# Kernel optimization log

Measured on AMD Instinct MI355X. Metric: run time of the kernel, lower is better.

Reference implementation:

```python
import jax, jax.numpy as jnp
import numpy as np

N_HEAD = 16
E = 1024
B, T = 2, 2048


def setup_inputs() -> dict:
    key = jax.random.key(0)
    ks = jax.random.split(key, 5)
    s = 1.0 / np.sqrt(E)
    return {
        "x": jax.random.normal(ks[0], (B, T, E), dtype=jnp.float32),
        "w_qkv": jax.random.normal(ks[1], (E, 3 * E), dtype=jnp.float32) * s,
        "b_qkv": jnp.zeros((3 * E,), dtype=jnp.float32),
        "w_proj": jax.random.normal(ks[2], (E, E), dtype=jnp.float32) * s,
        "b_proj": jnp.zeros((E,), dtype=jnp.float32),
    }


def reference(x, w_qkv, b_qkv, w_proj, b_proj):
    Bsz, Tlen, Emb = x.shape
    hd = Emb // N_HEAD
    qkv = x @ w_qkv + b_qkv  # [B, T, 3E]
    q, k, v = jnp.split(qkv, 3, axis=-1)
    # [B, H, T, hd]
    q = q.reshape(Bsz, Tlen, N_HEAD, hd).transpose(0, 2, 1, 3)
    k = k.reshape(Bsz, Tlen, N_HEAD, hd).transpose(0, 2, 1, 3)
    v = v.reshape(Bsz, Tlen, N_HEAD, hd).transpose(0, 2, 1, 3)
    scale = 1.0 / jnp.sqrt(jnp.asarray(hd, dtype=x.dtype))
    scores = jnp.einsum("bhqd,bhkd->bhqk", q, k) * scale  # [B, H, T, T]
    causal = jnp.tril(jnp.ones((Tlen, Tlen), dtype=bool))
    scores = jnp.where(causal, scores, jnp.asarray(-jnp.inf, dtype=scores.dtype))
    attn = jax.nn.softmax(scores, axis=-1)
    y = jnp.einsum("bhqk,bhkd->bhqd", attn, v)  # [B, H, T, hd]
    y = y.transpose(0, 2, 1, 3).reshape(Bsz, Tlen, Emb)
    return y @ w_proj + b_proj
```

## Files before the change

### kernel.cpp

```cpp
#include <hip/hip_runtime.h>
#include <hip/hip_bf16.h>

typedef __hip_bfloat16 bf16;
typedef __attribute__((ext_vector_type(8))) short sh8;
typedef __attribute__((ext_vector_type(4))) float f32x4;

#define BB 2
#define TT 2048
#define EE 1024
#define NH 16
#define HD 64
#define M_ROWS (BB * TT)
#define PPAD 72

__device__ __forceinline__ float b2f(bf16 v) { return __bfloat162float(v); }
__device__ __forceinline__ bf16 f2b(float v) { return __float2bfloat16(v); }
__device__ __forceinline__ unsigned short f2bu(float v) {
    union { bf16 b; unsigned short u; } x; x.b = f2b(v); return x.u;
}

__device__ __forceinline__ void gl2lds16(const bf16* g, bf16* l) {
    __builtin_amdgcn_global_load_lds(
        (__attribute__((address_space(1))) void*)g,
        (__attribute__((address_space(3))) void*)l, 16, 0, 0);
}

__global__ __launch_bounds__(256) void prep(
    const float* __restrict__ x, bf16* __restrict__ xb,
    const float* __restrict__ Wq, bf16* __restrict__ Wqt,
    const float* __restrict__ Wp, bf16* __restrict__ Wpt) {
    const int bid = blockIdx.x;
    if (bid < 4096) {
        const int i = bid * 256 + threadIdx.x;
        const float4 v = ((const float4*)x)[i];
        ushort4 u;
        u.x = f2bu(v.x); u.y = f2bu(v.y); u.z = f2bu(v.z); u.w = f2bu(v.w);
        ((ushort4*)xb)[i] = u;
        return;
    }
    __shared__ float Ld[64][65];
    const float* src; bf16* dst; int ncols, nc0, kr0;
    if (bid < 4096 + 768) {
        const int t = bid - 4096;
        src = Wq; dst = Wqt; ncols = 3072;
        nc0 = (t % 48) * 64; kr0 = (t / 48) * 64;
    } else {
        const int t = bid - 4096 - 768;
        src = Wp; dst = Wpt; ncols = 1024;
        nc0 = (t % 16) * 64; kr0 = (t / 16) * 64;
    }
#pragma unroll
    for (int i = 0; i < 16; ++i) {
        const int e = threadIdx.x + i * 256;
        Ld[e >> 6][e & 63] = src[(size_t)(kr0 + (e >> 6)) * ncols + nc0 + (e & 63)];
    }
    __syncthreads();
#pragma unroll
    for (int i = 0; i < 16; ++i) {
        const int e = threadIdx.x + i * 256;
        const int r2 = e & 63, c2 = e >> 6;
        dst[(size_t)(nc0 + c2) * EE + kr0 + r2] = f2b(Ld[r2][c2]);
    }
}

__device__ __forceinline__ void mfma_gemm_core(
    const bf16* __restrict__ A, const bf16* __restrict__ Bt,
    int m0, int n0, f32x4 acc[4][4], bf16* Al, bf16* Bl) {
    const int tid = threadIdx.x, w = tid >> 6, lane = tid & 63;
    const int li = lane & 15, quad = lane >> 4;
    const int wm = (w & 1) * 64, wn = (w >> 1) * 64;
    const int srow = w * 32 + (lane >> 3);
    const int scol = (lane & 7) * 8;

#pragma unroll
    for (int mt = 0; mt < 4; ++mt)
#pragma unroll
        for (int nt = 0; nt < 4; ++nt) acc[mt][nt] = (f32x4){0.f, 0.f, 0.f, 0.f};

    for (int k0 = 0; k0 < EE; k0 += 64) {
        __syncthreads();
#pragma unroll
        for (int j = 0; j < 4; ++j) {
            const int row = srow + j * 8;
            const int sk = scol ^ ((row & 7) * 8);
            gl2lds16(A  + (size_t)(m0 + row) * EE + k0 + sk, Al + row * 64 + scol);
            gl2lds16(Bt + (size_t)(n0 + row) * EE + k0 + sk, Bl + row * 64 + scol);
        }
        __syncthreads();
#pragma unroll
        for (int ks = 0; ks < 2; ++ks) {
            const int kof = (ks * 32 + quad * 8) ^ ((li & 7) * 8);
            sh8 af[4], bv[4];
#pragma unroll
            for (int mt = 0; mt < 4; ++mt)
                af[mt] = *(const sh8*)(Al + (wm + mt * 16 + li) * 64 + kof);
#pragma unroll
            for (int nt = 0; nt < 4; ++nt)
                bv[nt] = *(const sh8*)(Bl + (wn + nt * 16 + li) * 64 + kof);
#pragma unroll
            for (int mt = 0; mt < 4; ++mt)
#pragma unroll
                for (int nt = 0; nt < 4; ++nt)
                    acc[mt][nt] = __builtin_amdgcn_mfma_f32_16x16x32_bf16(
                        af[mt], bv[nt], acc[mt][nt], 0, 0, 0);
        }
    }
}

__global__ __launch_bounds__(256) void gemm_qkv_mfma(
    const bf16* __restrict__ A, const bf16* __restrict__ Bt,
    const float* __restrict__ bias,
    bf16* __restrict__ Qb, bf16* __restrict__ Kb, bf16* __restrict__ Vb) {
    __shared__ bf16 Al[128 * 64];
    __shared__ bf16 Bl[128 * 64];
    f32x4 acc[4][4];
    const int m0 = blockIdx.y * 128, n0 = blockIdx.x * 128;
    mfma_gemm_core(A, Bt, m0, n0, acc, Al, Bl);

    const int tid = threadIdx.x, w = tid >> 6, lane = tid & 63;
    const int li = lane & 15, quad = lane >> 4;
    const int wm = (w & 1) * 64, wn = (w >> 1) * 64;
    const int which = n0 >> 10;

#pragma unroll
    for (int nt = 0; nt < 4; ++nt) {
        const int n = n0 + wn + nt * 16 + li;
        const int hseg = n & 1023;
        const int h = hseg >> 6, d = hseg & 63;
        const float bv = bias[n];
        if (which == 2) {
#pragma unroll
            for (int mt = 0; mt < 4; ++mt) {
                const int mb = m0 + wm + mt * 16 + quad * 4;
                const int b = mb >> 11, t = mb & (TT - 1);
                ushort4 u;
                u.x = f2bu(acc[mt][nt][0] + bv);
                u.y = f2bu(acc[mt][nt][1] + bv);
                u.z = f2bu(acc[mt][nt][2] + bv);
                u.w = f2bu(acc[mt][nt][3] + bv);
                *(ushort4*)(Vb + ((size_t)((b * NH + h) * HD + d)) * TT + t) = u;
            }
        } else {
            bf16* dst = (which == 0) ? Qb : Kb;
            const float scl = (which == 0) ? 0.125f : 1.0f;
#pragma unroll
            for (int mt = 0; mt < 4; ++mt)
#pragma unroll
                for (int r = 0; r < 4; ++r) {
                    const int m = m0 + wm + mt * 16 + quad * 4 + r;
                    const int b = m >> 11, t = m & (TT - 1);
                    dst[((size_t)(b * NH + h) * TT + t) * HD + d] =
                        f2b((acc[mt][nt][r] + bv) * scl);
                }
        }
    }
}

__global__ __launch_bounds__(256) void gemm_proj_mfma(
    const bf16* __restrict__ A, const bf16* __restrict__ Bt,
    const float* __restrict__ bias, float* __restrict__ C) {
    __shared__ bf16 Al[128 * 64];
    __shared__ bf16 Bl[128 * 64];
    f32x4 acc[4][4];
    const int m0 = blockIdx.y * 128, n0 = blockIdx.x * 128;
    mfma_gemm_core(A, Bt, m0, n0, acc, Al, Bl);

    const int tid = threadIdx.x, w = tid >> 6, lane = tid & 63;
    const int li = lane & 15, quad = lane >> 4;
    const int wm = (w & 1) * 64, wn = (w >> 1) * 64;

#pragma unroll
    for (int nt = 0; nt < 4; ++nt) {
        const int n = n0 + wn + nt * 16 + li;
        const float bv = bias[n];
#pragma unroll
        for (int mt = 0; mt < 4; ++mt)
#pragma unroll
            for (int r = 0; r < 4; ++r) {
                const int m = m0 + wm + mt * 16 + quad * 4 + r;
                C[(size_t)m * EE + n] = acc[mt][nt][r] + bv;
            }
    }
}

__global__ __launch_bounds__(256) void attn_mfma(
    const bf16* __restrict__ Q, const bf16* __restrict__ K,
    const bf16* __restrict__ Vt, bf16* __restrict__ Y) {
    __shared__ bf16 Kl[2][64 * 64];
    __shared__ bf16 Vl[2][64 * 64];
    __shared__ bf16 Pl[4][16 * PPAD];

    const int tid  = threadIdx.x;
    const int w    = tid >> 6;
    const int lane = tid & 63;
    const int li   = lane & 15;
    const int quad = lane >> 4;
    const int swz  = (li & 7) * 8;
    const int idx  = blockIdx.x;
    const int qb   = 31 - (idx >> 5);
    const int bh   = idx & 31;
    const int q0   = qb << 6;
    const int qw0  = q0 + w * 16;

    const bf16* Qb = Q  + (size_t)bh * TT * HD;
    const bf16* Kb = K  + (size_t)bh * TT * HD;
    const bf16* Vb = Vt + (size_t)bh * HD * TT;

    sh8 qf0 = *(const sh8*)(Qb + (size_t)(qw0 + li) * HD + quad * 8);
    sh8 qf1 = *(const sh8*)(Qb + (size_t)(qw0 + li) * HD + 32 + quad * 8);

    f32x4 o[4];
#pragma unroll
    for (int nt = 0; nt < 4; ++nt) o[nt] = (f32x4){0.f, 0.f, 0.f, 0.f};
    float lacc = 0.f;

    const int l8 = lane >> 3, l7 = lane & 7;
    const int gcol = ((l7 ^ l8) * 8);

    const int ntiles = qb + 1;
#pragma unroll
    for (int c = 0; c < 2; ++c) {
        const int rb = w * 16 + c * 8;
        gl2lds16(Kb + (size_t)(rb + l8) * HD + gcol, &Kl[0][rb * 64]);
        gl2lds16(Vb + (size_t)(rb + l8) * TT + gcol, &Vl[0][rb * 64]);
    }

    for (int it = 0; it < ntiles; ++it) {
        const int cur = it & 1;
        __syncthreads();
        if (it + 1 < ntiles) {
            const int j1 = (it + 1) << 6;
            const int nxt = cur ^ 1;
#pragma unroll
            for (int c = 0; c < 2; ++c) {
                const int rb = w * 16 + c * 8;
                gl2lds16(Kb + (size_t)(j1 + rb + l8) * HD + gcol, &Kl[nxt][rb * 64]);
                gl2lds16(Vb + (size_t)(rb + l8) * TT + j1 + gcol, &Vl[nxt][rb * 64]);
            }
        }
        const bf16* kb = &Kl[cur][0];
        const bf16* vb = &Vl[cur][0];

        const bool diag = (it == ntiles - 1);
#pragma unroll
        for (int nt = 0; nt < 4; ++nt) {
            f32x4 a = (f32x4){0.f, 0.f, 0.f, 0.f};
            sh8 kf0 = *(const sh8*)(kb + (nt * 16 + li) * 64 + ((quad * 8) ^ swz));
            a = __builtin_amdgcn_mfma_f32_16x16x32_bf16(kf0, qf0, a, 0, 0, 0);
            sh8 kf1 = *(const sh8*)(kb + (nt * 16 + li) * 64 + ((32 + quad * 8) ^ swz));
            a = __builtin_amdgcn_mfma_f32_16x16x32_bf16(kf1, qf1, a, 0, 0, 0);

            ushort4 u;
            float p0, p1, p2, p3;
            if (diag) {
                const int keyb = q0 + nt * 16 + quad * 4;
                const int qg = qw0 + li;
                p0 = (keyb + 0 > qg) ? 0.f : __expf(a[0]);
                p1 = (keyb + 1 > qg) ? 0.f : __expf(a[1]);
                p2 = (keyb + 2 > qg) ? 0.f : __expf(a[2]);
                p3 = (keyb + 3 > qg) ? 0.f : __expf(a[3]);
            } else {
                p0 = __expf(a[0]); p1 = __expf(a[1]);
                p2 = __expf(a[2]); p3 = __expf(a[3]);
            }
            lacc += (p0 + p1) + (p2 + p3);
            u.x = f2bu(p0); u.y = f2bu(p1); u.z = f2bu(p2); u.w = f2bu(p3);
            *(ushort4*)(&Pl[w][li * PPAD + nt * 16 + quad * 4]) = u;
        }

#pragma unroll
        for (int ks = 0; ks < 2; ++ks) {
            sh8 pf = *(const sh8*)(&Pl[w][li * PPAD + ks * 32 + quad * 8]);
#pragma unroll
            for (int nt = 0; nt < 4; ++nt) {
                sh8 vf = *(const sh8*)(vb + (nt * 16 + li) * 64 +
                                       ((ks * 32 + quad * 8) ^ swz));
                o[nt] = __builtin_amdgcn_mfma_f32_16x16x32_bf16(pf, vf, o[nt], 0, 0, 0);
            }
        }
    }

    lacc += __shfl_xor(lacc, 16, 64);
    lacc += __shfl_xor(lacc, 32, 64);
    float rinv[4];
#pragma unroll
    for (int r = 0; r < 4; ++r)
        rinv[r] = 1.0f / __shfl(lacc, quad * 4 + r, 64);

    const int b = bh >> 4, h = bh & 15;
#pragma unroll
    for (int nt = 0; nt < 4; ++nt)
#pragma unroll
        for (int r = 0; r < 4; ++r) {
            const int q = qw0 + quad * 4 + r;
            Y[((size_t)(b * TT + q)) * EE + h * HD + nt * 16 + li] =
                f2b(o[nt][r] * rinv[r]);
        }
}

extern "C" void kernel_launch(void* const* d_in, const int* in_sizes, int n_in,
                              void* d_out, int out_size, void* d_ws, size_t ws_size,
                              hipStream_t stream) {
    const float* x      = (const float*)d_in[0];
    const float* w_qkv  = (const float*)d_in[1];
    const float* b_qkv  = (const float*)d_in[2];
    const float* w_proj = (const float*)d_in[3];
    const float* b_proj = (const float*)d_in[4];
    float* out = (float*)d_out;

    const size_t SZ = (size_t)M_ROWS * EE;
    bf16* Q   = (bf16*)d_ws;
    bf16* K   = Q + SZ;
    bf16* V   = K + SZ;
    bf16* XB  = V + SZ;
    bf16* WQT = XB + SZ;
    bf16* WPT = WQT + 3 * SZ / 4;
    bf16* Y   = XB;

    prep<<<dim3(4096 + 768 + 256), dim3(256), 0, stream>>>(
        x, XB, w_qkv, WQT, w_proj, WPT);

    gemm_qkv_mfma<<<dim3(24, 32), dim3(256), 0, stream>>>(XB, WQT, b_qkv, Q, K, V);

    attn_mfma<<<dim3((TT / 64) * (BB * NH)), dim3(256), 0, stream>>>(Q, K, V, Y);

    gemm_proj_mfma<<<dim3(8, 32), dim3(256), 0, stream>>>(Y, WPT, b_proj, out);
}
```

Measured before the change: 185.6 us.

## Software-pipeline attention PV with QK, swap MFMA operands for vectorized stores

In the attention kernel, the P·V MFMAs for the previous tile now run after the QK^T MFMAs of the current tile, before the exp/softmax of the current tile. This overlaps matrix work with transcendental math, and a third V LDS buffer keeps the delayed tile resident. MFMA operands are swapped in the QK/proj GEMMs and in P·V so each lane holds 4 consecutive columns, which allows ushort4/float4 vector stores and a per-lane row sum without shuffles. The cost is more LDS for the extra V buffer and more live registers.

After: 188.6 us. No clear change (+1.6%).

```diff
diff --git a/kernel.cpp b/kernel.cpp
--- a/kernel.cpp
+++ b/kernel.cpp
@@ -63,6 +63,7 @@
     }
 }
 
+template <bool SWAP>
 __device__ __forceinline__ void mfma_gemm_core(
     const bf16* __restrict__ A, const bf16* __restrict__ Bt,
     int m0, int n0, f32x4 acc[4][4], bf16* Al, bf16* Bl) {
@@ -100,9 +101,14 @@
 #pragma unroll
             for (int mt = 0; mt < 4; ++mt)
 #pragma unroll
-                for (int nt = 0; nt < 4; ++nt)
-                    acc[mt][nt] = __builtin_amdgcn_mfma_f32_16x16x32_bf16(
-                        af[mt], bv[nt], acc[mt][nt], 0, 0, 0);
+                for (int nt = 0; nt < 4; ++nt) {
+                    if (SWAP)
+                        acc[mt][nt] = __builtin_amdgcn_mfma_f32_16x16x32_bf16(
+                            bv[nt], af[mt], acc[mt][nt], 0, 0, 0);
+                    else
+                        acc[mt][nt] = __builtin_amdgcn_mfma_f32_16x16x32_bf16(
+                            af[mt], bv[nt], acc[mt][nt], 0, 0, 0);
+                }
         }
     }
 }
@@ -115,20 +121,19 @@
     __shared__ bf16 Bl[128 * 64];
     f32x4 acc[4][4];
     const int m0 = blockIdx.y * 128, n0 = blockIdx.x * 128;
-    mfma_gemm_core(A, Bt, m0, n0, acc, Al, Bl);
-
     const int tid = threadIdx.x, w = tid >> 6, lane = tid & 63;
     const int li = lane & 15, quad = lane >> 4;
     const int wm = (w & 1) * 64, wn = (w >> 1) * 64;
     const int which = n0 >> 10;
 
-#pragma unroll
-    for (int nt = 0; nt < 4; ++nt) {
-        const int n = n0 + wn + nt * 16 + li;
-        const int hseg = n & 1023;
-        const int h = hseg >> 6, d = hseg & 63;
-        const float bv = bias[n];
-        if (which == 2) {
+    if (which == 2) {
+        mfma_gemm_core<false>(A, Bt, m0, n0, acc, Al, Bl);
+#pragma unroll
+        for (int nt = 0; nt < 4; ++nt) {
+            const int n = n0 + wn + nt * 16 + li;
+            const int hseg = n & 1023;
+            const int h = hseg >> 6, d = hseg & 63;
+            const float bv = bias[n];
 #pragma unroll
             for (int mt = 0; mt < 4; ++mt) {
                 const int mb = m0 + wm + mt * 16 + quad * 4;
@@ -140,18 +145,28 @@
                 u.w = f2bu(acc[mt][nt][3] + bv);
                 *(ushort4*)(Vb + ((size_t)((b * NH + h) * HD + d)) * TT + t) = u;
             }
-        } else {
-            bf16* dst = (which == 0) ? Qb : Kb;
-            const float scl = (which == 0) ? 0.125f : 1.0f;
-#pragma unroll
-            for (int mt = 0; mt < 4; ++mt)
-#pragma unroll
-                for (int r = 0; r < 4; ++r) {
-                    const int m = m0 + wm + mt * 16 + quad * 4 + r;
-                    const int b = m >> 11, t = m & (TT - 1);
-                    dst[((size_t)(b * NH + h) * TT + t) * HD + d] =
-                        f2b((acc[mt][nt][r] + bv) * scl);
-                }
+        }
+    } else {
+        mfma_gemm_core<true>(A, Bt, m0, n0, acc, Al, Bl);
+        bf16* dst = (which == 0) ? Qb : Kb;
+        const float scl = (which == 0) ? 0.125f : 1.0f;
+#pragma unroll
+        for (int nt = 0; nt < 4; ++nt) {
+            const int n = n0 + wn + nt * 16 + quad * 4;
+            const float4 bq = *(const float4*)(bias + n);
+            const int hseg = n & 1023;
+            const int h = hseg >> 6, d = hseg & 63;
+#pragma unroll
+            for (int mt = 0; mt < 4; ++mt) {
+                const int m = m0 + wm + mt * 16 + li;
+                const int b = m >> 11, t = m & (TT - 1);
+                ushort4 u;
+                u.x = f2bu((acc[mt][nt][0] + bq.x) * scl);
+                u.y = f2bu((acc[mt][nt][1] + bq.y) * scl);
+                u.z = f2bu((acc[mt][nt][2] + bq.z) * scl);
+                u.w = f2bu((acc[mt][nt][3] + bq.w) * scl);
+                *(ushort4*)(dst + ((size_t)(b * NH + h) * TT + t) * HD + d) = u;
+            }
         }
     }
 }
@@ -163,7 +178,7 @@
     __shared__ bf16 Bl[128 * 64];
     f32x4 acc[4][4];
     const int m0 = blockIdx.y * 128, n0 = blockIdx.x * 128;
-    mfma_gemm_core(A, Bt, m0, n0, acc, Al, Bl);
+    mfma_gemm_core<true>(A, Bt, m0, n0, acc, Al, Bl);
 
     const int tid = threadIdx.x, w = tid >> 6, lane = tid & 63;
     const int li = lane & 15, quad = lane >> 4;
@@ -171,15 +186,18 @@
 
 #pragma unroll
     for (int nt = 0; nt < 4; ++nt) {
-        const int n = n0 + wn + nt * 16 + li;
-        const float bv = bias[n];
-#pragma unroll
-        for (int mt = 0; mt < 4; ++mt)
-#pragma unroll
-            for (int r = 0; r < 4; ++r) {
-                const int m = m0 + wm + mt * 16 + quad * 4 + r;
-                C[(size_t)m * EE + n] = acc[mt][nt][r] + bv;
-            }
+        const int n = n0 + wn + nt * 16 + quad * 4;
+        const float4 bq = *(const float4*)(bias + n);
+#pragma unroll
+        for (int mt = 0; mt < 4; ++mt) {
+            const int m = m0 + wm + mt * 16 + li;
+            float4 v;
+            v.x = acc[mt][nt][0] + bq.x;
+            v.y = acc[mt][nt][1] + bq.y;
+            v.z = acc[mt][nt][2] + bq.z;
+            v.w = acc[mt][nt][3] + bq.w;
+            *(float4*)(C + (size_t)m * EE + n) = v;
+        }
     }
 }
 
@@ -187,7 +205,7 @@
     const bf16* __restrict__ Q, const bf16* __restrict__ K,
     const bf16* __restrict__ Vt, bf16* __restrict__ Y) {
     __shared__ bf16 Kl[2][64 * 64];
-    __shared__ bf16 Vl[2][64 * 64];
+    __shared__ bf16 Vl[3][64 * 64];
     __shared__ bf16 Pl[4][16 * PPAD];
 
     const int tid  = threadIdx.x;
@@ -225,23 +243,26 @@
         gl2lds16(Vb + (size_t)(rb + l8) * TT + gcol, &Vl[0][rb * 64]);
     }
 
+    int vc = 0;
+    int vp = 2;
     for (int it = 0; it < ntiles; ++it) {
-        const int cur = it & 1;
+        const int curK = it & 1;
         __syncthreads();
         if (it + 1 < ntiles) {
             const int j1 = (it + 1) << 6;
-            const int nxt = cur ^ 1;
+            const int vn = (vc == 2) ? 0 : vc + 1;
 #pragma unroll
             for (int c = 0; c < 2; ++c) {
                 const int rb = w * 16 + c * 8;
-                gl2lds16(Kb + (size_t)(j1 + rb + l8) * HD + gcol, &Kl[nxt][rb * 64]);
-                gl2lds16(Vb + (size_t)(rb + l8) * TT + j1 + gcol, &Vl[nxt][rb * 64]);
-            }
-        }
-        const bf16* kb = &Kl[cur][0];
-        const bf16* vb = &Vl[cur][0];
-
-        const bool diag = (it == ntiles - 1);
+                gl2lds16(Kb + (size_t)(j1 + rb + l8) * HD + gcol,
+                         &Kl[curK ^ 1][rb * 64]);
+                gl2lds16(Vb + (size_t)(rb + l8) * TT + j1 + gcol,
+                         &Vl[vn][rb * 64]);
+            }
+        }
+        const bf16* kb = &Kl[curK][0];
+
+        f32x4 sacc[4];
 #pragma unroll
         for (int nt = 0; nt < 4; ++nt) {
             f32x4 a = (f32x4){0.f, 0.f, 0.f, 0.f};
@@ -249,25 +270,51 @@
             a = __builtin_amdgcn_mfma_f32_16x16x32_bf16(kf0, qf0, a, 0, 0, 0);
             sh8 kf1 = *(const sh8*)(kb + (nt * 16 + li) * 64 + ((32 + quad * 8) ^ swz));
             a = __builtin_amdgcn_mfma_f32_16x16x32_bf16(kf1, qf1, a, 0, 0, 0);
-
-            ushort4 u;
+            sacc[nt] = a;
+        }
+
+        if (it > 0) {
+            const bf16* vb = &Vl[vp][0];
+#pragma unroll
+            for (int ks = 0; ks < 2; ++ks) {
+                sh8 pf = *(const sh8*)(&Pl[w][li * PPAD + ks * 32 + quad * 8]);
+#pragma unroll
+                for (int nt = 0; nt < 4; ++nt) {
+                    sh8 vf = *(const sh8*)(vb + (nt * 16 + li) * 64 +
+                                           ((ks * 32 + quad * 8) ^ swz));
+                    o[nt] = __builtin_amdgcn_mfma_f32_16x16x32_bf16(
+                        vf, pf, o[nt], 0, 0, 0);
+                }
+            }
+        }
+
+        const bool diag = (it == ntiles - 1);
+#pragma unroll
+        for (int nt = 0; nt < 4; ++nt) {
             float p0, p1, p2, p3;
             if (diag) {
                 const int keyb = q0 + nt * 16 + quad * 4;
                 const int qg = qw0 + li;
-                p0 = (keyb + 0 > qg) ? 0.f : __expf(a[0]);
-                p1 = (keyb + 1 > qg) ? 0.f : __expf(a[1]);
-                p2 = (keyb + 2 > qg) ? 0.f : __expf(a[2]);
-                p3 = (keyb + 3 > qg) ? 0.f : __expf(a[3]);
+                p0 = (keyb + 0 > qg) ? 0.f : __expf(sacc[nt][0]);
+                p1 = (keyb + 1 > qg) ? 0.f : __expf(sacc[nt][1]);
+                p2 = (keyb + 2 > qg) ? 0.f : __expf(sacc[nt][2]);
+                p3 = (keyb + 3 > qg) ? 0.f : __expf(sacc[nt][3]);
             } else {
-                p0 = __expf(a[0]); p1 = __expf(a[1]);
-                p2 = __expf(a[2]); p3 = __expf(a[3]);
+                p0 = __expf(sacc[nt][0]); p1 = __expf(sacc[nt][1]);
+                p2 = __expf(sacc[nt][2]); p3 = __expf(sacc[nt][3]);
             }
             lacc += (p0 + p1) + (p2 + p3);
+            ushort4 u;
             u.x = f2bu(p0); u.y = f2bu(p1); u.z = f2bu(p2); u.w = f2bu(p3);
             *(ushort4*)(&Pl[w][li * PPAD + nt * 16 + quad * 4]) = u;
         }
 
+        vp = vc;
+        vc = (vc == 2) ? 0 : vc + 1;
+    }
+
+    {
+        const bf16* vb = &Vl[vp][0];
 #pragma unroll
         for (int ks = 0; ks < 2; ++ks) {
             sh8 pf = *(const sh8*)(&Pl[w][li * PPAD + ks * 32 + quad * 8]);
@@ -275,27 +322,28 @@
             for (int nt = 0; nt < 4; ++nt) {
                 sh8 vf = *(const sh8*)(vb + (nt * 16 + li) * 64 +
                                        ((ks * 32 + quad * 8) ^ swz));
-                o[nt] = __builtin_amdgcn_mfma_f32_16x16x32_bf16(pf, vf, o[nt], 0, 0, 0);
+                o[nt] = __builtin_amdgcn_mfma_f32_16x16x32_bf16(
+                    vf, pf, o[nt], 0, 0, 0);
             }
         }
     }
 
     lacc += __shfl_xor(lacc, 16, 64);
     lacc += __shfl_xor(lacc, 32, 64);
-    float rinv[4];
-#pragma unroll
-    for (int r = 0; r < 4; ++r)
-        rinv[r] = 1.0f / __shfl(lacc, quad * 4 + r, 64);
+    const float rinv = 1.0f / lacc;
 
     const int b = bh >> 4, h = bh & 15;
-#pragma unroll
-    for (int nt = 0; nt < 4; ++nt)
-#pragma unroll
-        for (int r = 0; r < 4; ++r) {
-            const int q = qw0 + quad * 4 + r;
-            Y[((size_t)(b * TT + q)) * EE + h * HD + nt * 16 + li] =
-                f2b(o[nt][r] * rinv[r]);
-        }
+    const int q = qw0 + li;
+    bf16* yrow = Y + (size_t)(b * TT + q) * EE + h * HD;
+#pragma unroll
+    for (int nt = 0; nt < 4; ++nt) {
+        ushort4 u;
+        u.x = f2bu(o[nt][0] * rinv);
+        u.y = f2bu(o[nt][1] * rinv);
+        u.z = f2bu(o[nt][2] * rinv);
+        u.w = f2bu(o[nt][3] * rinv);
+        *(ushort4*)(yrow + nt * 16 + quad * 4) = u;
+    }
 }
 
 extern "C" void kernel_launch(void* const* d_in, const int* in_sizes, int n_in,
```
